# Kernel tuning notes

Measured on AMD Instinct MI355X. Metric: run time of the kernel, lower is better.

The kernel has to match this reference:

```python
import jax, jax.numpy as jnp
import numpy as np

STRIDES = [8, 16, 32, 64, 128]
HW = [(100, 128), (50, 64), (25, 32), (13, 16), (7, 8)]
SCORE_THR = 0.05
IOU_THR = 0.6
MAX_DET = 1000
MAX_OUT = 100  # fixed pad size in _post_process


def _coords(h, w, stride):
    # FCOS coords_fmap2orig: center of each cell in original image coords
    sx = jnp.arange(w, dtype=jnp.float32) * stride + stride // 2
    sy = jnp.arange(h, dtype=jnp.float32) * stride + stride // 2
    yy, xx = jnp.meshgrid(sy, sx, indexing='ij')
    return jnp.stack([xx.reshape(-1), yy.reshape(-1)], axis=-1)  # [h*w, 2]


def _reshape_cat(feats):
    # list of [B,C,h,w] -> [B, sum(h*w), C]
    outs = [f.transpose(0, 2, 3, 1).reshape(f.shape[0], -1, f.shape[1]) for f in feats]
    return jnp.concatenate(outs, axis=1)


def _nms_single(scores, classes, boxes):
    # scores [N] (sorted desc), classes [N] int, boxes [N,4]; greedy DIoU-NMS
    N = scores.shape[0]
    valid = scores >= SCORE_THR
    # batched_nms: offset boxes by class so cross-class boxes never overlap
    max_coord = jnp.max(jnp.where(valid[:, None], boxes, -jnp.inf))
    offs = classes.astype(boxes.dtype) * (max_coord + 1.0)
    b = boxes + offs[:, None]
    x1, y1, x2, y2 = b[:, 0], b[:, 1], b[:, 2], b[:, 3]
    areas = (x2 - x1 + 1.0) * (y2 - y1 + 1.0)
    cx, cy = (x1 + x2) * 0.5, (y1 + y2) * 0.5
    xmin = jnp.maximum(x1[:, None], x1[None, :]); ymin = jnp.maximum(y1[:, None], y1[None, :])
    xmax = jnp.minimum(x2[:, None], x2[None, :]); ymax = jnp.minimum(y2[:, None], y2[None, :])
    inter = jnp.clip(xmax - xmin, 0) * jnp.clip(ymax - ymin, 0)
    iou = inter / (areas[:, None] + areas[None, :] - inter)
    inter_diag = (cx[:, None] - cx[None, :]) ** 2 + (cy[:, None] - cy[None, :]) ** 2
    oxmin = jnp.minimum(x1[:, None], x1[None, :]); oymin = jnp.minimum(y1[:, None], y1[None, :])
    oxmax = jnp.maximum(x2[:, None], x2[None, :]); oymax = jnp.maximum(y2[:, None], y2[None, :])
    outer_diag = (oxmax - oxmin) ** 2 + (oymax - oymin) ** 2
    diou = iou - inter_diag / jnp.maximum(outer_diag, 1e-12)
    idxs = jnp.arange(N)

    def body(i, keep):
        sup = keep[i] & (idxs > i) & (diou[i] > IOU_THR)
        return keep & (~sup)

    keep = jax.lax.fori_loop(0, N, body, valid)
    # kept boxes in descending-score order, padded with -2 to MAX_OUT
    rank = jnp.cumsum(keep) - 1
    pos = jnp.where(keep, jnp.minimum(rank, MAX_OUT), MAX_OUT)  # slot MAX_OUT is dumped
    out_s = jnp.full((MAX_OUT + 1,), -2.0, scores.dtype).at[pos].set(jnp.where(keep, scores, -2.0))[:MAX_OUT]
    out_c = jnp.full((MAX_OUT + 1,), -2, classes.dtype).at[pos].set(jnp.where(keep, classes, -2))[:MAX_OUT]
    out_b = jnp.full((MAX_OUT + 1, 4), -2.0, boxes.dtype).at[pos].set(jnp.where(keep[:, None], boxes, -2.0))[:MAX_OUT]
    return out_s, out_c, out_b


def _forward(cls_feats, reg_feats):
    cls_logits = _reshape_cat(cls_feats)          # [B, L, C]
    reg_preds = _reshape_cat(reg_feats)           # [B, L, 4]
    coords = jnp.concatenate([_coords(h, w, s) for (h, w), s in zip(HW, STRIDES)], axis=0)
    cls_preds = jax.nn.sigmoid(cls_logits)
    cls_scores = jnp.max(cls_preds, axis=-1)      # [B, L]
    cls_classes = jnp.argmax(cls_preds, axis=-1) + 1
    x1y1 = coords[None] - reg_preds[..., :2]
    x2y2 = coords[None] + reg_preds[..., 2:]
    boxes = jnp.concatenate([x1y1, x2y2], axis=-1)  # [B, L, 4]
    max_num = min(MAX_DET, cls_scores.shape[-1])
    topv, topi = jax.lax.top_k(cls_scores, max_num)  # sorted descending
    top_c = jnp.take_along_axis(cls_classes, topi, axis=1)
    top_b = jnp.take_along_axis(boxes, topi[..., None], axis=1)
    return jax.vmap(_nms_single)(topv, top_c, top_b)


def setup_inputs() -> dict:
    key = jax.random.key(0)
    ks = jax.random.split(key, 16)
    inp = {}
    C = 80
    for i, (h, w) in enumerate(HW):
        inp[f'cls{i}'] = jax.random.normal(ks[i], (16, C, h, w), dtype=jnp.float32)
        # ltrb offsets scaled so boxes are realistically sized and overlap
        inp[f'reg{i}'] = jax.random.uniform(ks[5 + i], (16, 4, h, w), dtype=jnp.float32) * 64.0
    inp['boxes_anchor'] = jax.random.normal(ks[10], (16, 100, 4), dtype=jnp.float32)
    inp['labels_anchor'] = jax.random.randint(ks[11], (16, 100), 0, 80)
    inp['score_anchor'] = jax.random.uniform(ks[12], (16, 100), dtype=jnp.float32)
    return inp


def reference(cls0, cls1, cls2, cls3, cls4, reg0, reg1, reg2, reg3, reg4,
              boxes_anchor, labels_anchor, score_anchor):
    # nms_anchor (boxes_anchor, labels_anchor, score_anchor) is consumed but
    # does not affect the output in the original forward.
    scores, classes, boxes = _forward([cls0, cls1, cls2, cls3, cls4],
                                      [reg0, reg1, reg2, reg3, reg4])
    return scores, classes, boxes
```

## Files before the change

### kernel.cpp

```cpp
#include <hip/hip_runtime.h>
#include <math.h>

typedef unsigned int u32;
typedef unsigned long long u64;

#define BB 16
#define NANCH 17064
#define NGRP 4266
#define NTOP 1000
#define NWORD 16
#define NOUT 100
#define NBIN 8192
#define NSPLIT 17

__device__ __forceinline__ u32 fmap(float v) {
    u32 u = __float_as_uint(v);
    return (u & 0x80000000u) ? ~u : (u | 0x80000000u);
}
__device__ __forceinline__ float funmap(u32 u) {
    u32 b = (u & 0x80000000u) ? (u & 0x7FFFFFFFu) : ~u;
    return __uint_as_float(b);
}

__global__ void __launch_bounds__(256) k_anchor(
        const float* __restrict__ c0, const float* __restrict__ c1,
        const float* __restrict__ c2, const float* __restrict__ c3,
        const float* __restrict__ c4,
        const float* __restrict__ r0, const float* __restrict__ r1,
        const float* __restrict__ r2, const float* __restrict__ r3,
        const float* __restrict__ r4,
        u32* __restrict__ akey, int* __restrict__ aclass,
        float* __restrict__ abox) {
    int tid = threadIdx.x;
    int b = blockIdx.y;
    int gt = blockIdx.x * 256 + tid;
    if (gt >= 4 * NGRP) return;
    int p = gt >> 2, cs = gt & 3;
    int a = p * 4;

    const float *cp, *rp;
    int loc, wl, h, stride, half;
    if (a < 12800)      { loc = a;         wl = 7; h = 100; stride = 8;   half = 4;  cp = c0; rp = r0; }
    else if (a < 16000) { loc = a - 12800; wl = 6; h = 50;  stride = 16;  half = 8;  cp = c1; rp = r1; }
    else if (a < 16800) { loc = a - 16000; wl = 5; h = 25;  stride = 32;  half = 16; cp = c2; rp = r2; }
    else if (a < 17008) { loc = a - 16800; wl = 4; h = 13;  stride = 64;  half = 32; cp = c3; rp = r3; }
    else                { loc = a - 17008; wl = 3; h = 7;   stride = 128; half = 64; cp = c4; rp = r4; }
    int y = loc >> wl, x = loc & ((1 << wl) - 1);
    int hw = h << wl, hwq = hw >> 2;

    const float4* cb4 = (const float4*)(cp + (size_t)b * 80 * hw +
                                        (size_t)cs * 20 * hw + loc);
    int cbase = cs * 20;
    float4 v = cb4[0];
    float m0 = v.x, m1 = v.y, m2 = v.z, m3 = v.w;
    int a0 = cbase, a1 = cbase, a2 = cbase, a3 = cbase;
#pragma unroll
    for (int c = 1; c < 20; ++c) {
        float4 u = cb4[(size_t)c * hwq];
        int cc = cbase + c;
        if (u.x > m0) { m0 = u.x; a0 = cc; }
        if (u.y > m1) { m1 = u.y; a1 = cc; }
        if (u.z > m2) { m2 = u.z; a2 = cc; }
        if (u.w > m3) { m3 = u.w; a3 = cc; }
    }
    {
        bool low = (cs & 1) == 0;
        float pm; int pa; bool tk;
        pm = __shfl_xor(m0, 1); pa = __shfl_xor(a0, 1);
        tk = low ? (m0 >= pm) : (m0 > pm); m0 = tk ? m0 : pm; a0 = tk ? a0 : pa;
        pm = __shfl_xor(m1, 1); pa = __shfl_xor(a1, 1);
        tk = low ? (m1 >= pm) : (m1 > pm); m1 = tk ? m1 : pm; a1 = tk ? a1 : pa;
        pm = __shfl_xor(m2, 1); pa = __shfl_xor(a2, 1);
        tk = low ? (m2 >= pm) : (m2 > pm); m2 = tk ? m2 : pm; a2 = tk ? a2 : pa;
        pm = __shfl_xor(m3, 1); pa = __shfl_xor(a3, 1);
        tk = low ? (m3 >= pm) : (m3 > pm); m3 = tk ? m3 : pm; a3 = tk ? a3 : pa;
    }
    {
        bool low = (cs & 2) == 0;
        float pm; int pa; bool tk;
        pm = __shfl_xor(m0, 2); pa = __shfl_xor(a0, 2);
        tk = low ? (m0 >= pm) : (m0 > pm); m0 = tk ? m0 : pm; a0 = tk ? a0 : pa;
        pm = __shfl_xor(m1, 2); pa = __shfl_xor(a1, 2);
        tk = low ? (m1 >= pm) : (m1 > pm); m1 = tk ? m1 : pm; a1 = tk ? a1 : pa;
        pm = __shfl_xor(m2, 2); pa = __shfl_xor(a2, 2);
        tk = low ? (m2 >= pm) : (m2 > pm); m2 = tk ? m2 : pm; a2 = tk ? a2 : pa;
        pm = __shfl_xor(m3, 2); pa = __shfl_xor(a3, 2);
        tk = low ? (m3 >= pm) : (m3 > pm); m3 = tk ? m3 : pm; a3 = tk ? a3 : pa;
    }
    if (cs == 0) {
        const float4* rb4 = (const float4*)(rp + (size_t)b * 4 * hw + loc);
        float4 gl = rb4[0], gt_ = rb4[hwq], gr = rb4[2 * hwq], gb = rb4[3 * hwq];

        int idx = b * NANCH + a;
        *(uint4*)(akey + idx) = make_uint4(fmap(m0), fmap(m1), fmap(m2), fmap(m3));
        *(int4*)(aclass + idx) = make_int4(a0 + 1, a1 + 1, a2 + 1, a3 + 1);
        float cy = (float)(y * stride + half);
        float cx0 = (float)(x * stride + half);
        float gls[4] = {gl.x, gl.y, gl.z, gl.w};
        float gts[4] = {gt_.x, gt_.y, gt_.z, gt_.w};
        float grs[4] = {gr.x, gr.y, gr.z, gr.w};
        float gbs[4] = {gb.x, gb.y, gb.z, gb.w};
#pragma unroll
        for (int k = 0; k < 4; ++k) {
            float cx = cx0 + (float)(k * stride);
            *(float4*)(abox + (size_t)(idx + k) * 4) =
                make_float4(cx - gls[k], cy - gts[k], cx + grs[k], cy + gbs[k]);
        }
    }
}

__global__ void __launch_bounds__(256) k_hist(const u32* __restrict__ akey,
                                              u32* __restrict__ ghist) {
    __shared__ u32 lh[NBIN];
    int b = blockIdx.y, s = blockIdx.x, t = threadIdx.x;
    for (int i = t; i < NBIN; i += 256) lh[i] = 0;
    __syncthreads();
    int base = s * 1024;
    int n = min(1024, NANCH - base);
    if (4 * t < n) {
        uint4 k4 = *(const uint4*)(akey + (size_t)b * NANCH + base + 4 * t);
        atomicAdd(&lh[k4.x >> 19], 1u);
        atomicAdd(&lh[k4.y >> 19], 1u);
        atomicAdd(&lh[k4.z >> 19], 1u);
        atomicAdd(&lh[k4.w >> 19], 1u);
    }
    __syncthreads();
    u32* gh = ghist + b * NBIN;
    for (int i = t; i < NBIN; i += 256) {
        u32 c = lh[i];
        if (c) atomicAdd(&gh[i], c);
    }
}

__global__ void __launch_bounds__(256) k_compact(const u32* __restrict__ akey,
                                                 const u32* __restrict__ ghist,
                                                 u32* __restrict__ ccnt,
                                                 u64* __restrict__ cand) {
    __shared__ u32 hist[NBIN];
    __shared__ u32 seg[256];
    __shared__ u32 Ts, lcnt, baseoff;
    int b = blockIdx.y, s = blockIdx.x, t = threadIdx.x;
    const u32* gh = ghist + b * NBIN;
    for (int i = t; i < NBIN; i += 256) hist[i] = gh[i];
    if (t == 0) lcnt = 0;
    __syncthreads();
    u32 sg = 0;
#pragma unroll
    for (int j = 0; j < 32; ++j) sg += hist[t * 32 + ((j + t) & 31)];
    seg[t] = sg;
    __syncthreads();
    if (t == 0) {
        u32 acc = 0;
        int Tv = 0;
        for (int g = 255; g >= 0; --g) {
            if (acc + seg[g] >= NTOP) {
                for (int bin = g * 32 + 31; bin >= g * 32; --bin) {
                    acc += hist[bin];
                    if (acc >= NTOP) { Tv = bin; break; }
                }
                break;
            }
            acc += seg[g];
        }
        Ts = (u32)Tv;
    }
    __syncthreads();
    u32 T = Ts;

    int base = s * 1024;
    int n = min(1024, NANCH - base);
    u32 kk[4]; u32 pos[4]; bool m[4] = {false, false, false, false};
    if (4 * t < n) {
        uint4 k4 = *(const uint4*)(akey + (size_t)b * NANCH + base + 4 * t);
        kk[0] = k4.x; kk[1] = k4.y; kk[2] = k4.z; kk[3] = k4.w;
#pragma unroll
        for (int i = 0; i < 4; ++i) {
            m[i] = (kk[i] >> 19) >= T;
            if (m[i]) pos[i] = atomicAdd(&lcnt, 1u);
        }
    }
    __syncthreads();
    if (t == 0) baseoff = atomicAdd(&ccnt[b], lcnt);
    __syncthreads();
    u32 bo = baseoff;
    u64* cb = cand + (size_t)b * NANCH;
#pragma unroll
    for (int i = 0; i < 4; ++i) {
        if (m[i])
            cb[bo + pos[i]] =
                ((u64)kk[i] << 32) | (u64)(0xFFFFFFFFu - (u32)(base + 4 * t + i));
    }
}

__global__ void __launch_bounds__(256) k_rank(
        const u64* __restrict__ cand, const u32* __restrict__ ccnt,
        const int* __restrict__ aclass, const float* __restrict__ abox,
        float* __restrict__ tscore, int* __restrict__ tclass,
        float* __restrict__ tbox, u32* __restrict__ maxcU) {
    __shared__ u64 tile[2048];
    int b = blockIdx.y, tid = threadIdx.x;
    int C = (int)ccnt[b];
    const u64* ck = cand + (size_t)b * NANCH;
    for (int base = blockIdx.x * 256; base < C; base += gridDim.x * 256) {
        int i = base + tid;
        bool have = i < C;
        u64 my = have ? ck[i] : 0ull;
        int rank = 0;
        for (int t0 = 0; t0 < C; t0 += 2048) {
            int nt = min(2048, C - t0);
            __syncthreads();
            for (int j = tid; j < nt; j += 256) tile[j] = ck[t0 + j];
            __syncthreads();
            int r0 = 0, r1 = 0, r2 = 0, r3 = 0, r4 = 0, r5 = 0, r6 = 0, r7 = 0;
            int j = 0;
            for (; j + 8 <= nt; j += 8) {
                u64 v0 = tile[j + 0], v1 = tile[j + 1];
                u64 v2 = tile[j + 2], v3 = tile[j + 3];
                u64 v4 = tile[j + 4], v5 = tile[j + 5];
                u64 v6 = tile[j + 6], v7 = tile[j + 7];
                r0 += v0 > my; r1 += v1 > my; r2 += v2 > my; r3 += v3 > my;
                r4 += v4 > my; r5 += v5 > my; r6 += v6 > my; r7 += v7 > my;
            }
            for (; j < nt; ++j) r0 += tile[j] > my;
            rank += ((r0 + r1) + (r2 + r3)) + ((r4 + r5) + (r6 + r7));
        }
        u32 mymax = 0;
        if (have && rank < NTOP) {
            u32 a = 0xFFFFFFFFu - (u32)(my & 0xFFFFFFFFull);
            int src = b * NANCH + (int)a;
            int dst = b * NTOP + rank;
            float logit = funmap((u32)(my >> 32));
            float sc = 1.0f / (1.0f + expf(-logit));
            float b0 = abox[src * 4 + 0], b1 = abox[src * 4 + 1];
            float b2 = abox[src * 4 + 2], b3 = abox[src * 4 + 3];
            tscore[dst] = sc;
            tclass[dst] = aclass[src];
            tbox[dst * 4 + 0] = b0;
            tbox[dst * 4 + 1] = b1;
            tbox[dst * 4 + 2] = b2;
            tbox[dst * 4 + 3] = b3;
            if (sc >= 0.05f)
                mymax = fmap(fmaxf(fmaxf(b0, b1), fmaxf(b2, b3)));
        }
        for (int off = 32; off > 0; off >>= 1) {
            u32 o = (u32)__shfl_down((int)mymax, off);
            mymax = mymax > o ? mymax : o;
        }
        if ((tid & 63) == 0) atomicMax(&maxcU[b], mymax);
    }
}

__global__ void k_sup(const float* __restrict__ tbox, const int* __restrict__ tclass,
                      const u32* __restrict__ maxcU, u64* __restrict__ sup) {
    int u = blockIdx.x, b = blockIdx.y;
    int ti = 0, rem = u;
    while (rem >= NWORD - ti) { rem -= NWORD - ti; ++ti; }
    int tj = ti + rem;
    int t = threadIdx.x;
    __shared__ double jx1[64], jy1[64], jx2[64], jy2[64], jcx[64], jcy[64], jar[64];
    double mc1 = (double)funmap(maxcU[b]) + 1.0;
    int j = tj * 64 + t;
    if (j < NTOP) {
        const float* bx = tbox + (size_t)(b * NTOP + j) * 4;
        double o = (double)tclass[b * NTOP + j] * mc1;
        double x1 = (double)bx[0] + o, y1 = (double)bx[1] + o;
        double x2 = (double)bx[2] + o, y2 = (double)bx[3] + o;
        jx1[t] = x1; jy1[t] = y1; jx2[t] = x2; jy2[t] = y2;
        jcx[t] = (x1 + x2) * 0.5; jcy[t] = (y1 + y2) * 0.5;
        jar[t] = (x2 - x1 + 1.0) * (y2 - y1 + 1.0);
    }
    __syncthreads();
    int i = ti * 64 + t;
    if (i >= NTOP) return;
    const float* bx = tbox + (size_t)(b * NTOP + i) * 4;
    double o = (double)tclass[b * NTOP + i] * mc1;
    double ix1 = (double)bx[0] + o, iy1 = (double)bx[1] + o;
    double ix2 = (double)bx[2] + o, iy2 = (double)bx[3] + o;
    double icx = (ix1 + ix2) * 0.5, icy = (iy1 + iy2) * 0.5;
    double iar = (ix2 - ix1 + 1.0) * (iy2 - iy1 + 1.0);
    u64 bits = 0;
    int jbase = tj * 64;
    for (int jj = 0; jj < 64; ++jj) {
        int jg = jbase + jj;
        if (jg >= NTOP) break;
        if (jg <= i) continue;
        double xm = fmax(ix1, jx1[jj]), ym = fmax(iy1, jy1[jj]);
        double xM = fmin(ix2, jx2[jj]), yM = fmin(iy2, jy2[jj]);
        double inter = fmax(xM - xm, 0.0) * fmax(yM - ym, 0.0);
        double iou = inter / (iar + jar[jj] - inter);
        double dx = icx - jcx[jj], dy = icy - jcy[jj];
        double idg = dx * dx + dy * dy;
        double ox = fmax(ix2, jx2[jj]) - fmin(ix1, jx1[jj]);
        double oy = fmax(iy2, jy2[jj]) - fmin(iy1, jy1[jj]);
        double odg = ox * ox + oy * oy;
        double diou = iou - idg / fmax(odg, 1e-12);
        if (diou > 0.6) bits |= (1ull << jj);
    }
    sup[(size_t)(b * NTOP + i) * NWORD + tj] = bits;
}

__global__ void __launch_bounds__(64) k_scan(
        const u64* __restrict__ sup, const float* __restrict__ tscore,
        const int* __restrict__ tclass, const float* __restrict__ tbox,
        float* __restrict__ out) {
    int b = blockIdx.x, lane = threadIdx.x;
    __shared__ u64 lds[64 * 17];
    __shared__ int kept_lds[NOUT];
    const u64* supb = sup + (size_t)b * NTOP * NWORD;
    u64 remw = 0;
    int kept = 0;
    for (int t = 0; t < NWORD; ++t) {
        int r0 = t * 64;
#pragma unroll
        for (int q = 0; q < 16; ++q) {
            int e = q * 64 + lane;
            int rr = r0 + (e >> 4), w = e & 15;
            u64 v = (rr < NTOP) ? supb[(size_t)rr * 16 + w] : 0ull;
            lds[(e >> 4) * 17 + w] = v;
        }
        __syncthreads();
        int r = r0 + lane;
        float s = (r < NTOP) ? tscore[b * NTOP + r] : -1.0f;
        u64 vmask = __ballot(s >= 0.05f);
        u64 M = lds[lane * 17 + t];
        u64 rem_t = __shfl(remw, t);
        u64 cnd = vmask & ~rem_t;
        u64 keepmask = 0;
        while (cnd) {
            int k = __ffsll(cnd) - 1;
            keepmask |= 1ull << k;
            if (lane == 0) kept_lds[kept] = r0 + k;
            ++kept;
            if (kept >= NOUT) break;
            u64 Mk = __shfl(M, k);
            cnd &= ~(Mk | (1ull << k));
        }
        if (lane < NWORD) {
            u64 km = keepmask;
            while (km) {
                int k = __ffsll(km) - 1;
                km &= km - 1;
                remw |= lds[k * 17 + lane];
            }
        }
        __syncthreads();
        if (kept >= NOUT) break;
    }
    float* os = out + b * NOUT;
    float* oc = out + BB * NOUT + b * NOUT;
    float* ob = out + 2 * BB * NOUT + (size_t)b * NOUT * 4;
    for (int i = lane; i < NOUT; i += 64) { os[i] = -2.0f; oc[i] = -2.0f; }
    for (int i = lane; i < NOUT * 4; i += 64) ob[i] = -2.0f;
    __syncthreads();
    int ncopy = kept < NOUT ? kept : NOUT;
    for (int r = lane; r < ncopy; r += 64) {
        int i = kept_lds[r];
        os[r] = tscore[b * NTOP + i];
        oc[r] = (float)tclass[b * NTOP + i];
        ob[r * 4 + 0] = tbox[(size_t)(b * NTOP + i) * 4 + 0];
        ob[r * 4 + 1] = tbox[(size_t)(b * NTOP + i) * 4 + 1];
        ob[r * 4 + 2] = tbox[(size_t)(b * NTOP + i) * 4 + 2];
        ob[r * 4 + 3] = tbox[(size_t)(b * NTOP + i) * 4 + 3];
    }
}

extern "C" void kernel_launch(void* const* d_in, const int* in_sizes, int n_in,
                              void* d_out, int out_size, void* d_ws, size_t ws_size,
                              hipStream_t stream) {
    (void)in_sizes; (void)n_in; (void)out_size; (void)ws_size;
    const float* cls[5];
    const float* reg[5];
    for (int i = 0; i < 5; ++i) {
        cls[i] = (const float*)d_in[2 * i];
        reg[i] = (const float*)d_in[2 * i + 1];
    }
    float* out = (float*)d_out;

    char* ws = (char*)d_ws;
    u32* ghist = (u32*)ws;           ws += (size_t)BB * NBIN * sizeof(u32);
    u32* ccnt = (u32*)ws;            ws += 64;
    u32* maxcU = (u32*)ws;           ws += 64;
    size_t zbytes = (size_t)BB * NBIN * sizeof(u32) + 128;
    u64* cand = (u64*)ws;            ws += (size_t)BB * NANCH * sizeof(u64);
    u64* sup = (u64*)ws;             ws += (size_t)BB * NTOP * NWORD * sizeof(u64);
    u32* akey = (u32*)ws;            ws += (size_t)BB * NANCH * sizeof(u32);
    int* aclass = (int*)ws;          ws += (size_t)BB * NANCH * sizeof(int);
    float* abox = (float*)ws;        ws += (size_t)BB * NANCH * 4 * sizeof(float);
    float* tscore = (float*)ws;      ws += (size_t)BB * NTOP * sizeof(float);
    int* tclass = (int*)ws;          ws += (size_t)BB * NTOP * sizeof(int);
    float* tbox = (float*)ws;        ws += (size_t)BB * NTOP * 4 * sizeof(float);

    hipMemsetAsync(ghist, 0, zbytes, stream);

    k_anchor<<<dim3((4 * NGRP + 255) / 256, BB), 256, 0, stream>>>(
        cls[0], cls[1], cls[2], cls[3], cls[4],
        reg[0], reg[1], reg[2], reg[3], reg[4],
        akey, aclass, abox);
    k_hist<<<dim3(NSPLIT, BB), 256, 0, stream>>>(akey, ghist);
    k_compact<<<dim3(NSPLIT, BB), 256, 0, stream>>>(akey, ghist, ccnt, cand);
    k_rank<<<dim3(14, BB), 256, 0, stream>>>(cand, ccnt, aclass, abox,
                                             tscore, tclass, tbox, maxcU);
    k_sup<<<dim3(136, BB), 64, 0, stream>>>(tbox, tclass, maxcU, sup);
    k_scan<<<BB, 64, 0, stream>>>(sup, tscore, tclass, tbox, out);
}
```

Before: 235.4 us.

## Fuse histogram into anchor kernel, widen bins, add parallel threshold-scan kernel

The anchor kernel now bumps a 65536-bin global histogram directly with atomics, so the separate histogram kernel goes away. A new per-batch kernel finds the top-1000 threshold with two parallel suffix scans, which lets the compact kernel skip loading the histogram and running a serial search. Finer bins should leave fewer candidates, so the rank kernel grid shrinks. The DIoU test is also rewritten without divisions. The costs are a larger memset, global atomic contention, and an inequality that may differ from the reference at edge cases.

```diff
diff --git a/kernel.cpp b/kernel.cpp
--- a/kernel.cpp
+++ b/kernel.cpp
@@ -10,7 +10,7 @@
 #define NTOP 1000
 #define NWORD 16
 #define NOUT 100
-#define NBIN 8192
+#define NBIN 65536
 #define NSPLIT 17
 
 __device__ __forceinline__ u32 fmap(float v) {
@@ -30,7 +30,7 @@
         const float* __restrict__ r2, const float* __restrict__ r3,
         const float* __restrict__ r4,
         u32* __restrict__ akey, int* __restrict__ aclass,
-        float* __restrict__ abox) {
+        float* __restrict__ abox, u32* __restrict__ ghist) {
     int tid = threadIdx.x;
     int b = blockIdx.y;
     int gt = blockIdx.x * 256 + tid;
@@ -92,8 +92,14 @@
         float4 gl = rb4[0], gt_ = rb4[hwq], gr = rb4[2 * hwq], gb = rb4[3 * hwq];
 
         int idx = b * NANCH + a;
-        *(uint4*)(akey + idx) = make_uint4(fmap(m0), fmap(m1), fmap(m2), fmap(m3));
+        u32 km0 = fmap(m0), km1 = fmap(m1), km2 = fmap(m2), km3 = fmap(m3);
+        *(uint4*)(akey + idx) = make_uint4(km0, km1, km2, km3);
         *(int4*)(aclass + idx) = make_int4(a0 + 1, a1 + 1, a2 + 1, a3 + 1);
+        u32* gh = ghist + (size_t)b * NBIN;
+        atomicAdd(&gh[km0 >> 16], 1u);
+        atomicAdd(&gh[km1 >> 16], 1u);
+        atomicAdd(&gh[km2 >> 16], 1u);
+        atomicAdd(&gh[km3 >> 16], 1u);
         float cy = (float)(y * stride + half);
         float cx0 = (float)(x * stride + half);
         float gls[4] = {gl.x, gl.y, gl.z, gl.w};
@@ -109,63 +115,58 @@
     }
 }
 
-__global__ void __launch_bounds__(256) k_hist(const u32* __restrict__ akey,
-                                              u32* __restrict__ ghist) {
-    __shared__ u32 lh[NBIN];
-    int b = blockIdx.y, s = blockIdx.x, t = threadIdx.x;
-    for (int i = t; i < NBIN; i += 256) lh[i] = 0;
-    __syncthreads();
-    int base = s * 1024;
-    int n = min(1024, NANCH - base);
-    if (4 * t < n) {
-        uint4 k4 = *(const uint4*)(akey + (size_t)b * NANCH + base + 4 * t);
-        atomicAdd(&lh[k4.x >> 19], 1u);
-        atomicAdd(&lh[k4.y >> 19], 1u);
-        atomicAdd(&lh[k4.z >> 19], 1u);
-        atomicAdd(&lh[k4.w >> 19], 1u);
-    }
-    __syncthreads();
-    u32* gh = ghist + b * NBIN;
-    for (int i = t; i < NBIN; i += 256) {
-        u32 c = lh[i];
-        if (c) atomicAdd(&gh[i], c);
-    }
+__global__ void __launch_bounds__(256) k_thresh(const u32* __restrict__ ghist,
+                                                u32* __restrict__ thr) {
+    __shared__ u32 seg[256];
+    __shared__ u32 binv[256];
+    __shared__ int Gmax, Tmax;
+    int b = blockIdx.x, t = threadIdx.x;
+    const u32* gh = ghist + (size_t)b * NBIN;
+    u32 s = 0;
+    const uint4* g4 = (const uint4*)(gh + t * 256);
+#pragma unroll 8
+    for (int j = 0; j < 64; ++j) {
+        uint4 q = g4[j];
+        s += q.x + q.y + q.z + q.w;
+    }
+    seg[t] = s;
+    if (t == 0) { Gmax = 0; }
+    __syncthreads();
+    for (int off = 1; off < 256; off <<= 1) {
+        u32 v = seg[t];
+        u32 add = (t + off < 256) ? seg[t + off] : 0u;
+        __syncthreads();
+        seg[t] = v + add;
+        __syncthreads();
+    }
+    if (seg[t] >= NTOP) atomicMax(&Gmax, t);
+    __syncthreads();
+    int G = Gmax;
+    u32 hi = (G < 255) ? seg[G + 1] : 0u;
+    binv[t] = gh[G * 256 + t];
+    if (t == 0) { Tmax = G * 256; }
+    __syncthreads();
+    for (int off = 1; off < 256; off <<= 1) {
+        u32 v = binv[t];
+        u32 add = (t + off < 256) ? binv[t + off] : 0u;
+        __syncthreads();
+        binv[t] = v + add;
+        __syncthreads();
+    }
+    if (binv[t] + hi >= NTOP) atomicMax(&Tmax, G * 256 + t);
+    __syncthreads();
+    if (t == 0) thr[b] = (u32)Tmax;
 }
 
 __global__ void __launch_bounds__(256) k_compact(const u32* __restrict__ akey,
-                                                 const u32* __restrict__ ghist,
+                                                 const u32* __restrict__ thr,
                                                  u32* __restrict__ ccnt,
                                                  u64* __restrict__ cand) {
-    __shared__ u32 hist[NBIN];
-    __shared__ u32 seg[256];
-    __shared__ u32 Ts, lcnt, baseoff;
+    __shared__ u32 lcnt, baseoff;
     int b = blockIdx.y, s = blockIdx.x, t = threadIdx.x;
-    const u32* gh = ghist + b * NBIN;
-    for (int i = t; i < NBIN; i += 256) hist[i] = gh[i];
     if (t == 0) lcnt = 0;
     __syncthreads();
-    u32 sg = 0;
-#pragma unroll
-    for (int j = 0; j < 32; ++j) sg += hist[t * 32 + ((j + t) & 31)];
-    seg[t] = sg;
-    __syncthreads();
-    if (t == 0) {
-        u32 acc = 0;
-        int Tv = 0;
-        for (int g = 255; g >= 0; --g) {
-            if (acc + seg[g] >= NTOP) {
-                for (int bin = g * 32 + 31; bin >= g * 32; --bin) {
-                    acc += hist[bin];
-                    if (acc >= NTOP) { Tv = bin; break; }
-                }
-                break;
-            }
-            acc += seg[g];
-        }
-        Ts = (u32)Tv;
-    }
-    __syncthreads();
-    u32 T = Ts;
+    u32 T = thr[b];
 
     int base = s * 1024;
     int n = min(1024, NANCH - base);
@@ -175,7 +176,7 @@
         kk[0] = k4.x; kk[1] = k4.y; kk[2] = k4.z; kk[3] = k4.w;
 #pragma unroll
         for (int i = 0; i < 4; ++i) {
-            m[i] = (kk[i] >> 19) >= T;
+            m[i] = (kk[i] >> 16) >= T;
             if (m[i]) pos[i] = atomicAdd(&lcnt, 1u);
         }
     }
@@ -287,14 +288,13 @@
         double xm = fmax(ix1, jx1[jj]), ym = fmax(iy1, jy1[jj]);
         double xM = fmin(ix2, jx2[jj]), yM = fmin(iy2, jy2[jj]);
         double inter = fmax(xM - xm, 0.0) * fmax(yM - ym, 0.0);
-        double iou = inter / (iar + jar[jj] - inter);
+        double U = iar + jar[jj] - inter;
         double dx = icx - jcx[jj], dy = icy - jcy[jj];
         double idg = dx * dx + dy * dy;
         double ox = fmax(ix2, jx2[jj]) - fmin(ix1, jx1[jj]);
         double oy = fmax(iy2, jy2[jj]) - fmin(iy1, jy1[jj]);
-        double odg = ox * ox + oy * oy;
-        double diou = iou - idg / fmax(odg, 1e-12);
-        if (diou > 0.6) bits |= (1ull << jj);
+        double odg = fmax(ox * ox + oy * oy, 1e-12);
+        if (inter * odg - idg * U > 0.6 * (U * odg)) bits |= (1ull << jj);
     }
     sup[(size_t)(b * NTOP + i) * NWORD + tj] = bits;
 }
@@ -381,6 +381,7 @@
     u32* ccnt = (u32*)ws;            ws += 64;
     u32* maxcU = (u32*)ws;           ws += 64;
     size_t zbytes = (size_t)BB * NBIN * sizeof(u32) + 128;
+    u32* thr = (u32*)ws;             ws += 64;
     u64* cand = (u64*)ws;            ws += (size_t)BB * NANCH * sizeof(u64);
     u64* sup = (u64*)ws;             ws += (size_t)BB * NTOP * NWORD * sizeof(u64);
     u32* akey = (u32*)ws;            ws += (size_t)BB * NANCH * sizeof(u32);
@@ -395,11 +396,11 @@
     k_anchor<<<dim3((4 * NGRP + 255) / 256, BB), 256, 0, stream>>>(
         cls[0], cls[1], cls[2], cls[3], cls[4],
         reg[0], reg[1], reg[2], reg[3], reg[4],
-        akey, aclass, abox);
-    k_hist<<<dim3(NSPLIT, BB), 256, 0, stream>>>(akey, ghist);
-    k_compact<<<dim3(NSPLIT, BB), 256, 0, stream>>>(akey, ghist, ccnt, cand);
-    k_rank<<<dim3(14, BB), 256, 0, stream>>>(cand, ccnt, aclass, abox,
-                                             tscore, tclass, tbox, maxcU);
+        akey, aclass, abox, ghist);
+    k_thresh<<<BB, 256, 0, stream>>>(ghist, thr);
+    k_compact<<<dim3(NSPLIT, BB), 256, 0, stream>>>(akey, thr, ccnt, cand);
+    k_rank<<<dim3(8, BB), 256, 0, stream>>>(cand, ccnt, aclass, abox,
+                                            tscore, tclass, tbox, maxcU);
     k_sup<<<dim3(136, BB), 64, 0, stream>>>(tbox, tclass, maxcU, sup);
     k_scan<<<BB, 64, 0, stream>>>(sup, tscore, tclass, tbox, out);
 }
```

Measured after the change: 268.9 us. 14.2% more time.
